# Kernel tuning notes

Measured on AMD Instinct MI355X. Metric: run time of the kernel, lower is better.

## Reference

```python
import jax, jax.numpy as jnp
import numpy as np

NUM_EMBEDDINGS = 100000
EMBED_DIM = 256
DEGREE = 3
BATCH = 1024
SEQ = 50


def _subtree_mask(dim, d):
    # M[j, i] = 1 iff node i is in the subtree rooted at j (tree with parent(i) = (i-1)//d).
    # The torch loop `for i in D-1..1: m[(i-1)//d] += m[i]` yields exactly m_out[j] = sum_{i in subtree(j)} m_in[i],
    # because children of j have indices d*j+1..d*j+d > j and are processed before j receives its add.
    M = np.zeros((dim, dim), dtype=np.float32)
    for i in range(dim):
        j = i
        M[j, i] = 1.0
        while j > 0:
            j = (j - 1) // d
            M[j, i] = 1.0
    return M

_M = jnp.asarray(_subtree_mask(EMBED_DIM, DEGREE))  # [D, D] static 0/1 mask


def setup_inputs() -> dict:
    key = jax.random.key(0)
    k_w, k_x, k_y = jax.random.split(key, 3)
    weight = jax.random.normal(k_w, (NUM_EMBEDDINGS, EMBED_DIM), dtype=jnp.float32)
    x = jax.random.randint(k_x, (BATCH, SEQ), 0, NUM_EMBEDDINGS, dtype=jnp.int64)
    y = jax.random.randint(k_y, (BATCH, SEQ), 0, NUM_EMBEDDINGS, dtype=jnp.int64)
    return {"weight": weight, "x": x, "y": y}


def _subtree_prob(weight, idx):
    # gather -> softmax over embedding dim -> child->parent cumulative tree sum
    p = jax.nn.softmax(weight[idx], axis=-1)            # [B, S, D]
    return jnp.einsum('bsd,kd->bsk', p, _M)             # [B, S, D] subtree-summed probs


def reference(weight, x, y):
    xs = _subtree_prob(weight, x)
    ys = _subtree_prob(weight, y)
    # L1 (tree) distance over embedding dim
    return jnp.sum(jnp.abs(xs - ys), axis=-1)           # [B, S]
```

## Files before the change

kernel.cpp:

```cpp
#include <hip/hip_runtime.h>

#define D 256
#define WAVES_PER_BLOCK 4

__device__ __forceinline__ void lds_fence() {
    asm volatile("s_waitcnt lgkmcnt(0)" ::: "memory");
    __builtin_amdgcn_sched_barrier(0);
}

template<int CTRL>
__device__ __forceinline__ float dpp0(float v) {
    return __int_as_float(__builtin_amdgcn_update_dpp(
        0, __float_as_int(v), CTRL, 0xF, 0xF, true));
}

__device__ __forceinline__ float wave_sum_dpp(float v) {
    v += dpp0<0x111>(v);
    v += dpp0<0x112>(v);
    v += dpp0<0x114>(v);
    v += dpp0<0x118>(v);
    v += dpp0<0x142>(v);
    v += dpp0<0x143>(v);
    return __int_as_float(__builtin_amdgcn_readlane(__float_as_int(v), 63));
}

__global__ __launch_bounds__(256) void poincare_tree_l1_kernel(
    const float* __restrict__ weight,
    const int*   __restrict__ xi,
    const int*   __restrict__ yi,
    float*       __restrict__ out,
    int npairs)
{
    __shared__ __align__(16) float sbuf[WAVES_PER_BLOCK][D];

    const int wave = threadIdx.x >> 6;
    const int lane = threadIdx.x & 63;
    const int pair = blockIdx.x * WAVES_PER_BLOCK + wave;
    const int p = pair < npairs ? pair : npairs - 1;

    const int ix = xi[p];
    const int iy = yi[p];

    const float4 ax = ((const float4*)(weight + (size_t)ix * D))[lane];
    const float4 ay = ((const float4*)(weight + (size_t)iy * D))[lane];

    const float ex0 = __expf(ax.x), ex1 = __expf(ax.y);
    const float ex2 = __expf(ax.z), ex3 = __expf(ax.w);
    const float ey0 = __expf(ay.x), ey1 = __expf(ay.y);
    const float ey2 = __expf(ay.z), ey3 = __expf(ay.w);

    const float invx = 1.0f / wave_sum_dpp((ex0 + ex1) + (ex2 + ex3));
    const float invy = 1.0f / wave_sum_dpp((ey0 + ey1) + (ey2 + ey3));

    const float d0 = ex0 * invx - ey0 * invy;
    const float d1 = ex1 * invx - ey1 * invy;
    const float d2 = ex2 * invx - ey2 * invy;
    const float d3 = ex3 * invx - ey3 * invy;

    float acc = 0.0f;
    if (lane >= 22) acc  = fabsf(d0);
    if (lane >= 21) acc += fabsf(d1) + fabsf(d2) + fabsf(d3);

    float* s = sbuf[wave];
    ((float4*)s)[lane] = make_float4(d0, d1, d2, d3);
    lds_fence();

    if (lane < 45) {
        const int j = 40 + lane;
        const float v = s[j] + s[3*j+1] + s[3*j+2] + s[3*j+3];
        s[j] = v; acc += fabsf(v);
    }
    lds_fence();
    if (lane < 27) {
        const int j = 13 + lane;
        const float v = s[j] + s[3*j+1] + s[3*j+2] + s[3*j+3];
        s[j] = v; acc += fabsf(v);
    }
    lds_fence();
    if (lane < 9) {
        const int j = 4 + lane;
        const float v = s[j] + s[3*j+1] + s[3*j+2] + s[3*j+3];
        s[j] = v; acc += fabsf(v);
    }
    lds_fence();
    if (lane < 3) {
        const int j = 1 + lane;
        const float v = s[j] + s[3*j+1] + s[3*j+2] + s[3*j+3];
        s[j] = v; acc += fabsf(v);
    }
    lds_fence();
    if (lane == 0) {
        const float v = s[0] + s[1] + s[2] + s[3];
        acc += fabsf(v);
    }

    const float total = wave_sum_dpp(acc);

    if (lane == 0 && pair < npairs) out[pair] = total;
}

extern "C" void kernel_launch(void* const* d_in, const int* in_sizes, int n_in,
                              void* d_out, int out_size, void* d_ws, size_t ws_size,
                              hipStream_t stream) {
    const float* weight = (const float*)d_in[0];
    const int*   xi     = (const int*)d_in[1];
    const int*   yi     = (const int*)d_in[2];
    float*       out    = (float*)d_out;

    const int npairs = out_size;
    const int blocks = (npairs + WAVES_PER_BLOCK - 1) / WAVES_PER_BLOCK;

    poincare_tree_l1_kernel<<<blocks, 256, 0, stream>>>(weight, xi, yi, out, npairs);
}
```

Baseline: 22.74 us.

## Compute subtree sums via wave prefix scan instead of level-by-level LDS passes

Replaces the four serialized LDS level reductions with a wave-wide inclusive prefix scan of the probability differences, written to LDS. Each subtree sum is then read as a difference of prefix values over contiguous index ranges per tree level. This removes several LDS round trips and fences from the dependency chain, at the cost of an extra DPP scan, padded LDS rows, and possible rounding differences from subtracting prefix sums.

```diff
diff --git a/kernel.cpp b/kernel.cpp
--- a/kernel.cpp
+++ b/kernel.cpp
@@ -2,26 +2,32 @@
 
 #define D 256
 #define WAVES_PER_BLOCK 4
+#define LDS_STRIDE 260
 
 __device__ __forceinline__ void lds_fence() {
     asm volatile("s_waitcnt lgkmcnt(0)" ::: "memory");
     __builtin_amdgcn_sched_barrier(0);
 }
 
-template<int CTRL>
-__device__ __forceinline__ float dpp0(float v) {
+template<int CTRL, int RM>
+__device__ __forceinline__ float dpp_term(float v) {
     return __int_as_float(__builtin_amdgcn_update_dpp(
-        0, __float_as_int(v), CTRL, 0xF, 0xF, true));
+        0, __float_as_int(v), CTRL, RM, 0xF, true));
+}
+
+__device__ __forceinline__ float wave_scan_incl(float v) {
+    v += dpp_term<0x111, 0xF>(v);
+    v += dpp_term<0x112, 0xF>(v);
+    v += dpp_term<0x114, 0xF>(v);
+    v += dpp_term<0x118, 0xF>(v);
+    v += dpp_term<0x142, 0xa>(v);
+    v += dpp_term<0x143, 0xc>(v);
+    return v;
 }
 
 __device__ __forceinline__ float wave_sum_dpp(float v) {
-    v += dpp0<0x111>(v);
-    v += dpp0<0x112>(v);
-    v += dpp0<0x114>(v);
-    v += dpp0<0x118>(v);
-    v += dpp0<0x142>(v);
-    v += dpp0<0x143>(v);
-    return __int_as_float(__builtin_amdgcn_readlane(__float_as_int(v), 63));
+    return __int_as_float(__builtin_amdgcn_readlane(
+        __float_as_int(wave_scan_incl(v)), 63));
 }
 
 __global__ __launch_bounds__(256) void poincare_tree_l1_kernel(
@@ -31,7 +37,7 @@
     float*       __restrict__ out,
     int npairs)
 {
-    __shared__ __align__(16) float sbuf[WAVES_PER_BLOCK][D];
+    __shared__ __align__(16) float sbuf[WAVES_PER_BLOCK][LDS_STRIDE];
 
     const int wave = threadIdx.x >> 6;
     const int lane = threadIdx.x & 63;
@@ -61,41 +67,38 @@
     if (lane >= 22) acc  = fabsf(d0);
     if (lane >= 21) acc += fabsf(d1) + fabsf(d2) + fabsf(d3);
 
+    const float local = (d0 + d1) + (d2 + d3);
+    const float incl  = wave_scan_incl(local);
+    const float base  = incl - local;
+    const float p1 = base + d0;
+    const float p2 = p1 + d1;
+    const float p3 = p2 + d2;
+
     float* s = sbuf[wave];
-    ((float4*)s)[lane] = make_float4(d0, d1, d2, d3);
+    ((float4*)s)[lane] = make_float4(base, p1, p2, p3);
+    if (lane == 63) s[D] = incl;
     lds_fence();
 
-    if (lane < 45) {
-        const int j = 40 + lane;
-        const float v = s[j] + s[3*j+1] + s[3*j+2] + s[3*j+3];
-        s[j] = v; acc += fabsf(v);
+    {
+        const int j = 21 + lane;
+        float sA = (s[j + 1] - s[j]) + (s[3 * j + 4] - s[3 * j + 1]);
+        if (j <= 27) sA += s[9 * j + 13] - s[9 * j + 4];
+        acc += fabsf(sA);
     }
-    lds_fence();
-    if (lane < 27) {
-        const int j = 13 + lane;
-        const float v = s[j] + s[3*j+1] + s[3*j+2] + s[3*j+3];
-        s[j] = v; acc += fabsf(v);
-    }
-    lds_fence();
-    if (lane < 9) {
-        const int j = 4 + lane;
-        const float v = s[j] + s[3*j+1] + s[3*j+2] + s[3*j+3];
-        s[j] = v; acc += fabsf(v);
-    }
-    lds_fence();
-    if (lane < 3) {
-        const int j = 1 + lane;
-        const float v = s[j] + s[3*j+1] + s[3*j+2] + s[3*j+3];
-        s[j] = v; acc += fabsf(v);
-    }
-    lds_fence();
-    if (lane == 0) {
-        const float v = s[0] + s[1] + s[2] + s[3];
-        acc += fabsf(v);
+    if (lane >= 1 && lane <= 20) {
+        const int j = lane;
+        float sB = (s[j + 1] - s[j]) + (s[3 * j + 4] - s[3 * j + 1])
+                 + (s[9 * j + 13] - s[9 * j + 4]);
+        if (j <= 8) sB += s[27 * j + 40] - s[27 * j + 13];
+        if (j <= 3) {
+            int a = 81 * j + 40;  if (a > 256) a = 256;
+            int b = 81 * j + 121; if (b > 256) b = 256;
+            sB += s[b] - s[a];
+        }
+        acc += fabsf(sB);
     }
 
     const float total = wave_sum_dpp(acc);
-
     if (lane == 0 && pair < npairs) out[pair] = total;
 }
 
```

Result: no change. 22.72 us (-0.1%).
